# Kernel tuning notes

Measured on AMD Instinct MI355X. Metric: run time of the kernel, lower is better.

Reference implementation:

```python
import jax, jax.numpy as jnp
import numpy as np

B, N, D, H, K_OUT, NCLUST = 8, 4096, 3, 256, 1024, 63


def setup_inputs() -> dict:
    key = jax.random.key(0)
    ks = jax.random.split(key, 16)

    def lin_w(k, out_d, in_d):
        return jax.random.normal(k, (out_d, in_d), jnp.float32) / np.float32(np.sqrt(in_d))

    def lin_b(k, out_d):
        return jax.random.normal(k, (out_d,), jnp.float32) * 0.01

    x = jax.random.normal(ks[0], (B, N, D), jnp.float32)
    # DBSCAN-style labels: -1 = noise, 0..NCLUST-1 cluster ids
    labels = jax.random.randint(ks[1], (B, N), -1, NCLUST)
    return {
        "x": x,
        "labels": labels,
        "Wq": lin_w(ks[2], D, D), "bq": lin_b(ks[3], D),
        "Wk": lin_w(ks[4], D, D), "bk": lin_b(ks[5], D),
        "Wv": lin_w(ks[6], D, D), "bv": lin_b(ks[7], D),
        "Wo": lin_w(ks[8], D, D), "bo": lin_b(ks[9], D),
        "W1": lin_w(ks[10], H, D), "b1": lin_b(ks[11], H),
        "W2": lin_w(ks[12], D, H), "b2": lin_b(ks[13], D),
    }


def reference(x, labels, Wq, bq, Wk, bk, Wv, bv, Wo, bo, W1, b1, W2, b2):
    # Projections are per-point linear maps; computing them on all points is
    # identical to per-cluster gathers in the original.
    q = x @ Wq.T + bq  # [B,N,D]
    k = x @ Wk.T + bk
    v = x @ Wv.T + bv

    scale = 1.0 / np.float32(np.sqrt(x.shape[-1]))  # SDPA default 1/sqrt(E)
    scores = jnp.einsum('bnd,bmd->bnm', q, k) * scale  # [B,N,N]

    valid = labels != -1  # noise points produce zero output
    # Block-diagonal mask: attend only within the same (non-noise) cluster.
    same = (labels[:, :, None] == labels[:, None, :]) & valid[:, :, None]
    scores = jnp.where(same, scores, jnp.float32(-1e9))
    attn = jax.nn.softmax(scores, axis=-1)
    ctx = jnp.einsum('bnm,bmd->bnd', attn, v)
    ctx = jnp.where(valid[:, :, None], ctx, 0.0)  # outputs stay zero for noise

    out = ctx @ Wo.T + bo  # out_proj applied to all rows (incl. zeroed noise rows)
    h = jax.nn.relu(out @ W1.T + b1)
    y = h @ W2.T + b2  # [B,N,D]
    return y[:, :K_OUT]  # stack of transformed[:K]
```

## Files before the change

kernel.cpp:

```cpp
#include <hip/hip_runtime.h>

#define BB 8
#define NN 4096
#define HH 256
#define KOUT 1024
#define NC 64
#define NSEG 16
#define SEG 256

__global__ __launch_bounds__(256) void k_build(
    const int* __restrict__ labels,
    int* __restrict__ counts,
    int* __restrict__ offs,
    int* __restrict__ members)
{
    int t = blockIdx.x * 256 + threadIdx.x;
    int b  = t >> 12;
    int sb = (t >> 8) & (NSEG - 1);
    int n  = t & (NN - 1);
    int l  = labels[t];

    __shared__ int hist[NC], cur[NC];
    if (threadIdx.x < NC) hist[threadIdx.x] = 0;
    __syncthreads();
    if (l >= 0) atomicAdd(&hist[l], 1);
    __syncthreads();
    if (threadIdx.x < NC) {
        int v = hist[threadIdx.x];
        int s = v;
        #pragma unroll
        for (int d = 1; d < 64; d <<= 1) {
            int o = __shfl_up(s, d, 64);
            if (threadIdx.x >= d) s += o;
        }
        int e = s - v;
        int gi = (b * NSEG + sb) * NC + threadIdx.x;
        counts[gi] = v;
        offs[gi]   = e;
        cur[threadIdx.x] = e;
    }
    __syncthreads();
    if (l >= 0) {
        int p = atomicAdd(&cur[l], 1);
        members[b * NN + sb * SEG + p] = n;
    }
}

__global__ __launch_bounds__(256) void k_attn(
    const float* __restrict__ x, const int* __restrict__ labels,
    const int* __restrict__ counts, const int* __restrict__ offs,
    const int* __restrict__ members,
    const float* __restrict__ Wq, const float* __restrict__ bq,
    const float* __restrict__ Wk, const float* __restrict__ bk,
    const float* __restrict__ Wv, const float* __restrict__ bv,
    const float* __restrict__ Wo, const float* __restrict__ bo,
    const float* __restrict__ W1, const float* __restrict__ b1,
    const float* __restrict__ W2, const float* __restrict__ b2,
    float* __restrict__ out)
{
    int row  = (blockIdx.x * 256 + threadIdx.x) >> 6;
    int lane = threadIdx.x & 63;
    int b = row >> 10, n = row & (KOUT - 1);
    int l = labels[b * NN + n];

    const float* xr = x + (b * NN + n) * 3;
    float x0 = xr[0], x1 = xr[1], x2 = xr[2];
    float q0 = bq[0] + x0 * Wq[0] + x1 * Wq[1] + x2 * Wq[2];
    float q1 = bq[1] + x0 * Wq[3] + x1 * Wq[4] + x2 * Wq[5];
    float q2 = bq[2] + x0 * Wq[6] + x1 * Wq[7] + x2 * Wq[8];

    float c0 = 0.f, c1 = 0.f, c2 = 0.f;
    if (l >= 0) {
        const float scale = 0.5773502691896258f;
        int s16 = lane & (NSEG - 1);
        int gi = (b * NSEG + s16) * NC + l;
        int cs = counts[gi];
        int start = b * NN + s16 * SEG + offs[gi];
        int p = cs;
        #pragma unroll
        for (int d = 1; d < 16; d <<= 1) {
            int o = __shfl_up(p, d, 16);
            if (s16 >= d) p += o;
        }
        int e = p - cs;
        int T = __shfl(p, 15, 64);

        float dsum = 0.f;
        int iters = (T + 63) >> 6;
        for (int it = 0; it < iters; ++it) {
            int i = lane + (it << 6);
            bool act = i < T;
            int ic = act ? i : (T - 1);
            int lo = 0;
            #pragma unroll
            for (int step = 8; step >= 1; step >>= 1) {
                int cand = lo + step;
                int ev = __shfl(e, cand, 64);
                lo = (ev <= ic) ? cand : lo;
            }
            int eo  = __shfl(e, lo, 64);
            int bse = __shfl(start, lo, 64);
            int m = members[bse + (ic - eo)];
            const float* xm = x + (b * NN + m) * 3;
            float y0 = xm[0], y1 = xm[1], y2 = xm[2];
            float k0 = bk[0] + y0 * Wk[0] + y1 * Wk[1] + y2 * Wk[2];
            float k1 = bk[1] + y0 * Wk[3] + y1 * Wk[4] + y2 * Wk[5];
            float k2 = bk[2] + y0 * Wk[6] + y1 * Wk[7] + y2 * Wk[8];
            float sc = (q0 * k0 + q1 * k1 + q2 * k2) * scale;
            float w = act ? __expf(sc) : 0.f;
            float v0 = bv[0] + y0 * Wv[0] + y1 * Wv[1] + y2 * Wv[2];
            float v1 = bv[1] + y0 * Wv[3] + y1 * Wv[4] + y2 * Wv[5];
            float v2 = bv[2] + y0 * Wv[6] + y1 * Wv[7] + y2 * Wv[8];
            dsum += w; c0 += w * v0; c1 += w * v1; c2 += w * v2;
        }
        #pragma unroll
        for (int d = 32; d > 0; d >>= 1) {
            dsum += __shfl_xor(dsum, d, 64);
            c0   += __shfl_xor(c0, d, 64);
            c1   += __shfl_xor(c1, d, 64);
            c2   += __shfl_xor(c2, d, 64);
        }
        float inv = 1.f / dsum;
        c0 *= inv; c1 *= inv; c2 *= inv;
    }

    float o0 = bo[0] + c0 * Wo[0] + c1 * Wo[1] + c2 * Wo[2];
    float o1 = bo[1] + c0 * Wo[3] + c1 * Wo[4] + c2 * Wo[5];
    float o2 = bo[2] + c0 * Wo[6] + c1 * Wo[7] + c2 * Wo[8];

    float y0 = 0.f, y1 = 0.f, y2 = 0.f;
    #pragma unroll
    for (int t = 0; t < 4; t++) {
        int j = lane + 64 * t;
        float h = fmaxf(W1[j * 3 + 0] * o0 + W1[j * 3 + 1] * o1 + W1[j * 3 + 2] * o2 + b1[j], 0.f);
        y0 += h * W2[j];
        y1 += h * W2[HH + j];
        y2 += h * W2[2 * HH + j];
    }
    #pragma unroll
    for (int d = 32; d > 0; d >>= 1) {
        y0 += __shfl_xor(y0, d, 64);
        y1 += __shfl_xor(y1, d, 64);
        y2 += __shfl_xor(y2, d, 64);
    }
    if (lane == 0) {
        out[row * 3 + 0] = y0 + b2[0];
        out[row * 3 + 1] = y1 + b2[1];
        out[row * 3 + 2] = y2 + b2[2];
    }
}

extern "C" void kernel_launch(void* const* d_in, const int* in_sizes, int n_in,
                              void* d_out, int out_size, void* d_ws, size_t ws_size,
                              hipStream_t stream) {
    const float* x      = (const float*)d_in[0];
    const int*   labels = (const int*)d_in[1];
    const float* Wq = (const float*)d_in[2];
    const float* bq = (const float*)d_in[3];
    const float* Wk = (const float*)d_in[4];
    const float* bk = (const float*)d_in[5];
    const float* Wv = (const float*)d_in[6];
    const float* bv = (const float*)d_in[7];
    const float* Wo = (const float*)d_in[8];
    const float* bo = (const float*)d_in[9];
    const float* W1 = (const float*)d_in[10];
    const float* b1 = (const float*)d_in[11];
    const float* W2 = (const float*)d_in[12];
    const float* b2 = (const float*)d_in[13];
    float* out = (float*)d_out;

    int* counts  = (int*)d_ws;
    int* offs    = counts + BB * NSEG * NC;
    int* members = offs + BB * NSEG * NC;

    k_build<<<(BB * NN) / 256, 256, 0, stream>>>(labels, counts, offs, members);
    k_attn<<<(BB * KOUT * 64) / 256, 256, 0, stream>>>(x, labels, counts, offs, members,
                                                       Wq, bq, Wk, bk, Wv, bv,
                                                       Wo, bo, W1, b1, W2, b2, out);
}
```

Measured before the change: 93.38 us.

## Precompute K/V into contiguous cluster-sorted buffers and drop segmented member lookup

The build kernel now runs one block per batch, builds a single per-cluster prefix offset, and writes projected K and V vectors (float4) in cluster-sorted order. The attention kernel then reads K/V contiguously for its cluster. This removes the 16-segment binary search, the indirect member gather, and the per-pair K/V projection recompute. It uses exp2 with a pre-folded log2e scale. The cost is a build kernel with only 8 blocks, which serialises histogram atomics on few CUs, and more workspace memory.

```diff
diff --git a/kernel.cpp b/kernel.cpp
--- a/kernel.cpp
+++ b/kernel.cpp
@@ -5,54 +5,82 @@
 #define HH 256
 #define KOUT 1024
 #define NC 64
-#define NSEG 16
-#define SEG 256
 
-__global__ __launch_bounds__(256) void k_build(
-    const int* __restrict__ labels,
-    int* __restrict__ counts,
-    int* __restrict__ offs,
-    int* __restrict__ members)
+__global__ __launch_bounds__(1024) void k_build(
+    const float* __restrict__ x, const int* __restrict__ labels,
+    const float* __restrict__ Wk, const float* __restrict__ bk,
+    const float* __restrict__ Wv, const float* __restrict__ bv,
+    int* __restrict__ cstart,
+    int* __restrict__ ccount,
+    float4* __restrict__ kp,
+    float4* __restrict__ vp)
 {
-    int t = blockIdx.x * 256 + threadIdx.x;
-    int b  = t >> 12;
-    int sb = (t >> 8) & (NSEG - 1);
-    int n  = t & (NN - 1);
-    int l  = labels[t];
+    int b   = blockIdx.x;
+    int tid = threadIdx.x;
+    __shared__ int hist[NC], cur[NC];
+    if (tid < NC) hist[tid] = 0;
+    __syncthreads();
 
-    __shared__ int hist[NC], cur[NC];
-    if (threadIdx.x < NC) hist[threadIdx.x] = 0;
+    int ls[4];
+#pragma unroll
+    for (int i = 0; i < 4; ++i) {
+        int l = labels[b * NN + tid + 1024 * i];
+        ls[i] = l;
+        if (l >= 0) atomicAdd(&hist[l], 1);
+    }
     __syncthreads();
-    if (l >= 0) atomicAdd(&hist[l], 1);
-    __syncthreads();
-    if (threadIdx.x < NC) {
-        int v = hist[threadIdx.x];
+
+    if (tid < NC) {
+        int v = hist[tid];
         int s = v;
-        #pragma unroll
+#pragma unroll
         for (int d = 1; d < 64; d <<= 1) {
             int o = __shfl_up(s, d, 64);
-            if (threadIdx.x >= d) s += o;
+            if (tid >= d) s += o;
         }
         int e = s - v;
-        int gi = (b * NSEG + sb) * NC + threadIdx.x;
-        counts[gi] = v;
-        offs[gi]   = e;
-        cur[threadIdx.x] = e;
+        cstart[b * NC + tid] = e;
+        ccount[b * NC + tid] = v;
+        cur[tid] = e;
     }
     __syncthreads();
-    if (l >= 0) {
+
+    float a0 = Wk[0], a1 = Wk[1], a2 = Wk[2];
+    float a3 = Wk[3], a4 = Wk[4], a5 = Wk[5];
+    float a6 = Wk[6], a7 = Wk[7], a8 = Wk[8];
+    float kb0 = bk[0], kb1 = bk[1], kb2 = bk[2];
+    float g0 = Wv[0], g1 = Wv[1], g2 = Wv[2];
+    float g3 = Wv[3], g4 = Wv[4], g5 = Wv[5];
+    float g6 = Wv[6], g7 = Wv[7], g8 = Wv[8];
+    float vb0 = bv[0], vb1 = bv[1], vb2 = bv[2];
+
+#pragma unroll
+    for (int i = 0; i < 4; ++i) {
+        int l = ls[i];
+        if (l < 0) continue;
+        int n = tid + 1024 * i;
         int p = atomicAdd(&cur[l], 1);
-        members[b * NN + sb * SEG + p] = n;
+        const float* xr = x + (b * NN + n) * 3;
+        float x0 = xr[0], x1 = xr[1], x2 = xr[2];
+        float4 kk, vv;
+        kk.x = kb0 + x0 * a0 + x1 * a1 + x2 * a2;
+        kk.y = kb1 + x0 * a3 + x1 * a4 + x2 * a5;
+        kk.z = kb2 + x0 * a6 + x1 * a7 + x2 * a8;
+        kk.w = 0.f;
+        vv.x = vb0 + x0 * g0 + x1 * g1 + x2 * g2;
+        vv.y = vb1 + x0 * g3 + x1 * g4 + x2 * g5;
+        vv.z = vb2 + x0 * g6 + x1 * g7 + x2 * g8;
+        vv.w = 0.f;
+        kp[b * NN + p] = kk;
+        vp[b * NN + p] = vv;
     }
 }
 
 __global__ __launch_bounds__(256) void k_attn(
     const float* __restrict__ x, const int* __restrict__ labels,
-    const int* __restrict__ counts, const int* __restrict__ offs,
-    const int* __restrict__ members,
+    const int* __restrict__ cstart, const int* __restrict__ ccount,
+    const float4* __restrict__ kp, const float4* __restrict__ vp,
     const float* __restrict__ Wq, const float* __restrict__ bq,
-    const float* __restrict__ Wk, const float* __restrict__ bk,
-    const float* __restrict__ Wv, const float* __restrict__ bv,
     const float* __restrict__ Wo, const float* __restrict__ bo,
     const float* __restrict__ W1, const float* __restrict__ b1,
     const float* __restrict__ W2, const float* __restrict__ b2,
@@ -71,49 +99,23 @@
 
     float c0 = 0.f, c1 = 0.f, c2 = 0.f;
     if (l >= 0) {
-        const float scale = 0.5773502691896258f;
-        int s16 = lane & (NSEG - 1);
-        int gi = (b * NSEG + s16) * NC + l;
-        int cs = counts[gi];
-        int start = b * NN + s16 * SEG + offs[gi];
-        int p = cs;
-        #pragma unroll
-        for (int d = 1; d < 16; d <<= 1) {
-            int o = __shfl_up(p, d, 16);
-            if (s16 >= d) p += o;
+        const float sl2e = 0.5773502691896258f * 1.4426950408889634f;
+        float qs0 = q0 * sl2e, qs1 = q1 * sl2e, qs2 = q2 * sl2e;
+
+        int T    = ccount[b * NC + l];
+        int base = b * NN + cstart[b * NC + l];
+        float dsum = 0.f;
+        int Tpad = (T + 63) & ~63;
+        for (int i = lane; i < Tpad; i += 64) {
+            bool act = i < T;
+            int idx = base + (act ? i : 0);
+            float4 kk = kp[idx];
+            float sc = qs0 * kk.x + qs1 * kk.y + qs2 * kk.z;
+            float w = act ? __builtin_amdgcn_exp2f(sc) : 0.f;
+            float4 vv = vp[idx];
+            dsum += w; c0 += w * vv.x; c1 += w * vv.y; c2 += w * vv.z;
         }
-        int e = p - cs;
-        int T = __shfl(p, 15, 64);
-
-        float dsum = 0.f;
-        int iters = (T + 63) >> 6;
-        for (int it = 0; it < iters; ++it) {
-            int i = lane + (it << 6);
-            bool act = i < T;
-            int ic = act ? i : (T - 1);
-            int lo = 0;
-            #pragma unroll
-            for (int step = 8; step >= 1; step >>= 1) {
-                int cand = lo + step;
-                int ev = __shfl(e, cand, 64);
-                lo = (ev <= ic) ? cand : lo;
-            }
-            int eo  = __shfl(e, lo, 64);
-            int bse = __shfl(start, lo, 64);
-            int m = members[bse + (ic - eo)];
-            const float* xm = x + (b * NN + m) * 3;
-            float y0 = xm[0], y1 = xm[1], y2 = xm[2];
-            float k0 = bk[0] + y0 * Wk[0] + y1 * Wk[1] + y2 * Wk[2];
-            float k1 = bk[1] + y0 * Wk[3] + y1 * Wk[4] + y2 * Wk[5];
-            float k2 = bk[2] + y0 * Wk[6] + y1 * Wk[7] + y2 * Wk[8];
-            float sc = (q0 * k0 + q1 * k1 + q2 * k2) * scale;
-            float w = act ? __expf(sc) : 0.f;
-            float v0 = bv[0] + y0 * Wv[0] + y1 * Wv[1] + y2 * Wv[2];
-            float v1 = bv[1] + y0 * Wv[3] + y1 * Wv[4] + y2 * Wv[5];
-            float v2 = bv[2] + y0 * Wv[6] + y1 * Wv[7] + y2 * Wv[8];
-            dsum += w; c0 += w * v0; c1 += w * v1; c2 += w * v2;
-        }
-        #pragma unroll
+#pragma unroll
         for (int d = 32; d > 0; d >>= 1) {
             dsum += __shfl_xor(dsum, d, 64);
             c0   += __shfl_xor(c0, d, 64);
@@ -129,7 +131,7 @@
     float o2 = bo[2] + c0 * Wo[6] + c1 * Wo[7] + c2 * Wo[8];
 
     float y0 = 0.f, y1 = 0.f, y2 = 0.f;
-    #pragma unroll
+#pragma unroll
     for (int t = 0; t < 4; t++) {
         int j = lane + 64 * t;
         float h = fmaxf(W1[j * 3 + 0] * o0 + W1[j * 3 + 1] * o1 + W1[j * 3 + 2] * o2 + b1[j], 0.f);
@@ -137,7 +139,7 @@
         y1 += h * W2[HH + j];
         y2 += h * W2[2 * HH + j];
     }
-    #pragma unroll
+#pragma unroll
     for (int d = 32; d > 0; d >>= 1) {
         y0 += __shfl_xor(y0, d, 64);
         y1 += __shfl_xor(y1, d, 64);
@@ -169,12 +171,14 @@
     const float* b2 = (const float*)d_in[13];
     float* out = (float*)d_out;
 
-    int* counts  = (int*)d_ws;
-    int* offs    = counts + BB * NSEG * NC;
-    int* members = offs + BB * NSEG * NC;
+    float4* kp     = (float4*)d_ws;
+    float4* vp     = kp + BB * NN;
+    int*    cstart = (int*)(vp + BB * NN);
+    int*    ccount = cstart + BB * NC;
 
-    k_build<<<(BB * NN) / 256, 256, 0, stream>>>(labels, counts, offs, members);
-    k_attn<<<(BB * KOUT * 64) / 256, 256, 0, stream>>>(x, labels, counts, offs, members,
-                                                       Wq, bq, Wk, bk, Wv, bv,
-                                                       Wo, bo, W1, b1, W2, b2, out);
+    k_build<<<BB, 1024, 0, stream>>>(x, labels, Wk, bk, Wv, bv,
+                                     cstart, ccount, kp, vp);
+    k_attn<<<(BB * KOUT * 64) / 256, 256, 0, stream>>>(x, labels, cstart, ccount,
+                                                       kp, vp, Wq, bq, Wo, bo,
+                                                       W1, b1, W2, b2, out);
 }
```

Measured after the change: 95.58 us. 2.4% more time.
